# Performance work log

Measured on AMD Instinct MI355X. Metric: run time of the kernel, lower is better.

The kernel has to match this reference:

```python
import jax, jax.numpy as jnp
import numpy as np


def _window_indices(L, K):
    # 0-based (emo, cau) index pairs kept in the torch flattening order:
    # emo varies slowly (outer), cau varies fast (inner), |cau-emo| <= K.
    i = np.repeat(np.arange(L), L)
    j = np.tile(np.arange(L), L)
    m = np.abs(j - i) <= K
    return i[m], j[m]


def setup_inputs() -> dict:
    key = jax.random.key(0)
    ks = jax.random.split(key, 6)
    B, L, D = 4, 512, 768
    K, P = 10, 50
    R = 2 * D + P  # rank_feat_dim = 1586
    return {
        "doc_sents_h": jax.random.normal(ks[0], (B, L, D), jnp.float32),
        "pos_emb": jax.random.normal(ks[1], (2 * K + 1, P), jnp.float32) * 0.05,
        "W1": jax.random.normal(ks[2], (R, R), jnp.float32) * (1.0 / np.sqrt(R)),
        "b1": jax.random.normal(ks[3], (R,), jnp.float32) * 0.01,
        "W2": jax.random.normal(ks[4], (R, 1), jnp.float32) * (1.0 / np.sqrt(R)),
        "b2": jax.random.normal(ks[5], (1,), jnp.float32) * 0.01,
    }


def reference(doc_sents_h, pos_emb, W1, b1, W2, b2):
    B, L, D = doc_sents_h.shape
    K = (pos_emb.shape[0] - 1) // 2
    ei, ci = _window_indices(L, K)           # static numpy, shape [n]
    rel = jnp.asarray(ci - ei)               # [n] in [-K, K]
    # windowed pair features, [B, n, 2D] (skips the O(L^2) materialization)
    P_pairs = jnp.concatenate([doc_sents_h[:, ei], doc_sents_h[:, ci]], axis=-1)
    emb = pos_emb[rel + K]                   # [n, pos_dim]
    relf = rel.astype(pos_emb.dtype)
    kernel = jnp.exp(-jnp.square(relf[:, None] - relf[None, :]))  # [n, n]
    emb = kernel @ emb                       # [n, pos_dim], batch-invariant
    couples = jnp.concatenate(
        [P_pairs, jnp.broadcast_to(emb, (B,) + emb.shape)], axis=-1)  # [B, n, R]
    h = jax.nn.relu(couples @ W1 + b1)       # [B, n, R]
    pred = (h @ W2 + b2)[..., 0]             # [B, n]
    emo_cau_pos = jnp.stack(
        [jnp.asarray(ei) + 1, jnp.asarray(ci) + 1], axis=1)  # [n, 2], 1-based
    return pred, emo_cau_pos, h
```

## Files before the change

kernel.cpp:

```cpp
#include <hip/hip_runtime.h>
#include <math.h>

#define B_   4
#define L_   512
#define D_   768
#define K_   10
#define P_   50
#define R_   1586
#define NP_  10642
#define MROWS 2048
#define NPAD 1664
#define UVS  1600

#define PRED_OFF 0
#define POS_OFF  (B_ * NP_)
#define H_OFF    (B_ * NP_ + NP_ * 2)

typedef __attribute__((ext_vector_type(8))) short short8;
typedef __attribute__((ext_vector_type(4))) float floatx4;

__device__ __forceinline__ unsigned short f2bf(float f) {
    union { float f; unsigned int u; } a; a.f = f;
    unsigned int u = a.u;
    return (unsigned short)((u + 0x7FFF + ((u >> 16) & 1)) >> 16);
}
__device__ __forceinline__ float bf2f(unsigned short u) {
    union { unsigned int u; float f; } a; a.u = ((unsigned int)u) << 16;
    return a.f;
}

__device__ __forceinline__ int pair_offset(int i) {
    int h = i < K_ ? i : K_;
    int off = h * (K_ + 1) + (h * (h - 1)) / 2;
    if (i > K_) {
        int fullEnd = i < (L_ - K_) ? i : (L_ - K_);
        off += (fullEnd - K_) * (2 * K_ + 1);
        if (i > L_ - K_) {
            int t = i - (L_ - K_);
            int first = 2 * K_;
            int last = L_ + K_ - (i - 1);
            off += (first + last) * t / 2;
        }
    }
    return off;
}

#define CA_BLOCKS 1536
#define CW_BLOCKS 2496
__global__ __launch_bounds__(256) void prep(
        const float* __restrict__ doc, const float* __restrict__ pos_emb,
        const float* __restrict__ W1, const float* __restrict__ b1,
        unsigned short* __restrict__ At, unsigned short* __restrict__ Wt,
        unsigned short* __restrict__ Fb) {
    __shared__ float tile[32][33];
    __shared__ float Es[P_];
    const int bid = blockIdx.x;

    if (bid < CA_BLOCKS) {
        int idx = (bid * 256 + threadIdx.x) * 4;
        float4 v = *(const float4*)(doc + idx);
        ushort4 o;
        o.x = f2bf(v.x); o.y = f2bf(v.y); o.z = f2bf(v.z); o.w = f2bf(v.w);
        *(ushort4*)(At + idx) = o;
        return;
    }
    if (bid < CA_BLOCKS + CW_BLOCKS) {
        int bb = bid - CA_BLOCKS;
        int z = bb / 1248, rem = bb % 1248;
        int k0 = (rem % 24) * 32;
        int n0 = (rem / 24) * 32;
        int tx = threadIdx.x & 31, ty = threadIdx.x >> 5;
        #pragma unroll
        for (int r = 0; r < 4; ++r) {
            int k = k0 + ty + r * 8;
            int n = n0 + tx;
            tile[ty + r * 8][tx] = (n < R_) ? W1[(size_t)(z * D_ + k) * R_ + n] : 0.f;
        }
        __syncthreads();
        #pragma unroll
        for (int r = 0; r < 4; ++r) {
            int n = n0 + ty + r * 8;
            int k = k0 + tx;
            Wt[(size_t)z * NPAD * D_ + (size_t)n * D_ + k] = f2bf(tile[tx][ty + r * 8]);
        }
        return;
    }
    int s = bid - (CA_BLOCKS + CW_BLOCKS);
    if (threadIdx.x < P_) {
        float acc = 0.f;
        #pragma unroll
        for (int r = 0; r <= 2 * K_; ++r) {
            float cnt = (float)(L_ - (r > K_ ? r - K_ : K_ - r));
            float d = (float)(s - r);
            acc += cnt * expf(-d * d) * pos_emb[r * P_ + threadIdx.x];
        }
        Es[threadIdx.x] = acc;
    }
    __syncthreads();
    for (int j = threadIdx.x; j < R_; j += 256) {
        float acc = b1[j];
        #pragma unroll 10
        for (int p = 0; p < P_; ++p)
            acc += Es[p] * W1[(2 * D_ + p) * R_ + j];
        Fb[s * UVS + j] = f2bf(acc);
    }
}

#define GLOAD_LDS16(g, l) __builtin_amdgcn_global_load_lds( \
    (const __attribute__((address_space(1))) void*)(g), \
    (__attribute__((address_space(3))) void*)(l), 16, 0, 0)

__global__ __launch_bounds__(256) void gemm_mfma(
        const unsigned short* __restrict__ At,
        const unsigned short* __restrict__ Wt,
        unsigned short* __restrict__ U, unsigned short* __restrict__ V) {
    __shared__ unsigned short Alds[128 * 32];
    __shared__ unsigned short Blds[128 * 32];
    const int tileN = blockIdx.x * 128;
    const int tileM = blockIdx.y * 128;
    const unsigned short* Bt = Wt + (size_t)blockIdx.z * NPAD * D_;
    unsigned short* C = blockIdx.z ? V : U;

    const int lane = threadIdx.x & 63;
    const int w = threadIdx.x >> 6;
    const int wm = (w & 1) * 64, wn = (w >> 1) * 64;
    const int quad = lane >> 4, l16 = lane & 15;

    floatx4 acc[4][4] = {};

    for (int k0 = 0; k0 < D_; k0 += 32) {
        #pragma unroll
        for (int t = 0; t < 2; ++t) {
            int g = (t * 4 + w) * 64 + lane;
            int m = g >> 2, c = g & 3;
            GLOAD_LDS16(At + (size_t)(tileM + m) * D_ + k0 + c * 8,
                        Alds + (t * 4 + w) * 512);
            GLOAD_LDS16(Bt + (size_t)(tileN + m) * D_ + k0 + c * 8,
                        Blds + (t * 4 + w) * 512);
        }
        __syncthreads();
        short8 a[4], b[4];
        #pragma unroll
        for (int im = 0; im < 4; ++im)
            a[im] = *(const short8*)&Alds[(wm + im * 16 + l16) * 32 + quad * 8];
        #pragma unroll
        for (int in = 0; in < 4; ++in)
            b[in] = *(const short8*)&Blds[(wn + in * 16 + l16) * 32 + quad * 8];
        #pragma unroll
        for (int im = 0; im < 4; ++im)
            #pragma unroll
            for (int in = 0; in < 4; ++in)
                acc[im][in] = __builtin_amdgcn_mfma_f32_16x16x32_bf16(
                    a[im], b[in], acc[im][in], 0, 0, 0);
        __syncthreads();
    }
    #pragma unroll
    for (int im = 0; im < 4; ++im) {
        #pragma unroll
        for (int in = 0; in < 4; ++in) {
            int col = tileN + wn + in * 16 + l16;
            if (col < R_) {
                #pragma unroll
                for (int r = 0; r < 4; ++r) {
                    int row = tileM + wm + im * 16 + quad * 4 + r;
                    C[(size_t)row * UVS + col] = f2bf(acc[im][in][r]);
                }
            }
        }
    }
}

#define NC2 13
__global__ __launch_bounds__(256) void epilogue(
        const unsigned short* __restrict__ U, const unsigned short* __restrict__ V,
        const unsigned short* __restrict__ Fb, const float* __restrict__ W2,
        const float* __restrict__ b2, float* __restrict__ out) {
    const int w    = threadIdx.x >> 6;
    const int lane = threadIdx.x & 63;
    const int b    = blockIdx.x >> 9;
    const int i    = blockIdx.x & (L_ - 1);

    const ushort2* u2  = (const ushort2*)(U + (size_t)(b * L_ + i) * UVS);
    const float2*  w2v = (const float2*)W2;

    float2 ur[NC2], wr[NC2];
    #pragma unroll
    for (int t = 0; t < NC2; ++t) {
        int c = lane + t * 64;
        if (c < R_ / 2) {
            ushort2 uu = u2[c];
            ur[t] = make_float2(bf2f(uu.x), bf2f(uu.y));
            wr[t] = w2v[c];
        }
    }

    const int base = i - K_ > 0 ? i - K_ : 0;
    const int poff = pair_offset(i);
    const float bias = b2[0];

    for (int dj = w; dj < 2 * K_ + 1; dj += 4) {
        int j = i - K_ + dj;
        if ((unsigned)j >= L_) continue;
        int p = poff + (j - base);
        const ushort2* v2 = (const ushort2*)(V + (size_t)(b * L_ + j) * UVS);
        const ushort2* f2 = (const ushort2*)(Fb + (size_t)dj * UVS);
        double* h2 = (double*)(out + H_OFF + (size_t)(b * NP_ + p) * R_);

        float acc = 0.f;
        #pragma unroll
        for (int t = 0; t < NC2; ++t) {
            int c = lane + t * 64;
            if (c < R_ / 2) {
                ushort2 vv = v2[c], ff = f2[c];
                float h0 = fmaxf(ur[t].x + bf2f(vv.x) + bf2f(ff.x), 0.f);
                float h1 = fmaxf(ur[t].y + bf2f(vv.y) + bf2f(ff.y), 0.f);
                union { float2 f; double d; } pk;
                pk.f = make_float2(h0, h1);
                __builtin_nontemporal_store(pk.d, h2 + c);
                acc += h0 * wr[t].x + h1 * wr[t].y;
            }
        }
        #pragma unroll
        for (int off = 32; off; off >>= 1) acc += __shfl_down(acc, off, 64);
        if (lane == 0) {
            out[PRED_OFF + b * NP_ + p] = acc + bias;
            if (b == 0) {
                out[POS_OFF + p * 2 + 0] = (float)(i + 1);
                out[POS_OFF + p * 2 + 1] = (float)(j + 1);
            }
        }
    }
}

extern "C" void kernel_launch(void* const* d_in, const int* in_sizes, int n_in,
                              void* d_out, int out_size, void* d_ws, size_t ws_size,
                              hipStream_t stream) {
    const float* doc     = (const float*)d_in[0];
    const float* pos_emb = (const float*)d_in[1];
    const float* W1      = (const float*)d_in[2];
    const float* b1      = (const float*)d_in[3];
    const float* W2      = (const float*)d_in[4];
    const float* b2      = (const float*)d_in[5];
    float* out = (float*)d_out;

    char* ws = (char*)d_ws;
    size_t off = 0;
    unsigned short* U  = (unsigned short*)(ws + off); off += (size_t)MROWS * UVS * 2;
    unsigned short* V  = (unsigned short*)(ws + off); off += (size_t)MROWS * UVS * 2;
    unsigned short* Fb = (unsigned short*)(ws + off); off += (size_t)21 * UVS * 2;
    off = (off + 255) & ~(size_t)255;
    unsigned short* At = (unsigned short*)(ws + off); off += (size_t)MROWS * D_ * 2;
    off = (off + 255) & ~(size_t)255;
    unsigned short* Wt = (unsigned short*)(ws + off);

    prep<<<CA_BLOCKS + CW_BLOCKS + 21, 256, 0, stream>>>(
        doc, pos_emb, W1, b1, At, Wt, Fb);
    gemm_mfma<<<dim3(NPAD / 128, MROWS / 128, 2), 256, 0, stream>>>(At, Wt, U, V);
    epilogue<<<dim3(MROWS), 256, 0, stream>>>(U, V, Fb, W2, b2, out);
}
```

Before: 361.1 us.

## Double-buffer LDS tiles in MFMA GEMM to overlap global loads with compute

The GEMM kernel now uses two LDS buffers for the A and B tiles. It issues the global-to-LDS loads for the next K-step before running the MFMAs on the current one, using explicit vmcnt waits and barriers. This is meant to hide global memory latency behind the matrix math instead of stalling on every K iteration. In exchange it doubles LDS use per block, which may lower occupancy, and it depends on hand-written waitcnt counts being correct.

```diff
diff --git a/kernel.cpp b/kernel.cpp
--- a/kernel.cpp
+++ b/kernel.cpp
@@ -114,8 +114,8 @@
         const unsigned short* __restrict__ At,
         const unsigned short* __restrict__ Wt,
         unsigned short* __restrict__ U, unsigned short* __restrict__ V) {
-    __shared__ unsigned short Alds[128 * 32];
-    __shared__ unsigned short Blds[128 * 32];
+    __shared__ unsigned short Alds[2][128 * 32];
+    __shared__ unsigned short Blds[2][128 * 32];
     const int tileN = blockIdx.x * 128;
     const int tileM = blockIdx.y * 128;
     const unsigned short* Bt = Wt + (size_t)blockIdx.z * NPAD * D_;
@@ -128,32 +128,51 @@
 
     floatx4 acc[4][4] = {};
 
-    for (int k0 = 0; k0 < D_; k0 += 32) {
-        #pragma unroll
-        for (int t = 0; t < 2; ++t) {
-            int g = (t * 4 + w) * 64 + lane;
-            int m = g >> 2, c = g & 3;
-            GLOAD_LDS16(At + (size_t)(tileM + m) * D_ + k0 + c * 8,
-                        Alds + (t * 4 + w) * 512);
-            GLOAD_LDS16(Bt + (size_t)(tileN + m) * D_ + k0 + c * 8,
-                        Blds + (t * 4 + w) * 512);
-        }
-        __syncthreads();
-        short8 a[4], b[4];
-        #pragma unroll
-        for (int im = 0; im < 4; ++im)
-            a[im] = *(const short8*)&Alds[(wm + im * 16 + l16) * 32 + quad * 8];
-        #pragma unroll
-        for (int in = 0; in < 4; ++in)
-            b[in] = *(const short8*)&Blds[(wn + in * 16 + l16) * 32 + quad * 8];
-        #pragma unroll
-        for (int im = 0; im < 4; ++im)
-            #pragma unroll
-            for (int in = 0; in < 4; ++in)
-                acc[im][in] = __builtin_amdgcn_mfma_f32_16x16x32_bf16(
-                    a[im], b[in], acc[im][in], 0, 0, 0);
-        __syncthreads();
-    }
+#define STAGE(buf, kk) do { \
+        _Pragma("unroll") \
+        for (int t = 0; t < 2; ++t) { \
+            int g = (t * 4 + w) * 64 + lane; \
+            int m = g >> 2, c = g & 3; \
+            GLOAD_LDS16(At + (size_t)(tileM + m) * D_ + (kk) + c * 8, \
+                        &Alds[buf][(t * 4 + w) * 512]); \
+            GLOAD_LDS16(Bt + (size_t)(tileN + m) * D_ + (kk) + c * 8, \
+                        &Blds[buf][(t * 4 + w) * 512]); \
+        } } while (0)
+
+#define KSTEP(rb, kk, dopf) do { \
+        if (dopf) { \
+            STAGE(rb ^ 1, (kk) + 32); \
+            asm volatile("s_waitcnt vmcnt(4)" ::: "memory"); \
+        } else { \
+            asm volatile("s_waitcnt vmcnt(0)" ::: "memory"); \
+        } \
+        __builtin_amdgcn_s_barrier(); \
+        __builtin_amdgcn_sched_barrier(0); \
+        short8 a[4], b[4]; \
+        _Pragma("unroll") \
+        for (int im = 0; im < 4; ++im) \
+            a[im] = *(const short8*)&Alds[rb][(wm + im * 16 + l16) * 32 + quad * 8]; \
+        _Pragma("unroll") \
+        for (int in = 0; in < 4; ++in) \
+            b[in] = *(const short8*)&Blds[rb][(wn + in * 16 + l16) * 32 + quad * 8]; \
+        _Pragma("unroll") \
+        for (int im = 0; im < 4; ++im) \
+            _Pragma("unroll") \
+            for (int in = 0; in < 4; ++in) \
+                acc[im][in] = __builtin_amdgcn_mfma_f32_16x16x32_bf16( \
+                    a[im], b[in], acc[im][in], 0, 0, 0); \
+        __builtin_amdgcn_sched_barrier(0); \
+        __builtin_amdgcn_s_barrier(); \
+    } while (0)
+
+    STAGE(0, 0);
+    for (int k0 = 0; k0 < D_; k0 += 64) {
+        KSTEP(0, k0, true);
+        KSTEP(1, k0 + 32, (k0 + 64) < D_);
+    }
+#undef KSTEP
+#undef STAGE
+
     #pragma unroll
     for (int im = 0; im < 4; ++im) {
         #pragma unroll
```

New measurement: 363.6 us. No clear change (+0.7%).

## Fuse prep, GEMM and epilogue into one cooperative persistent kernel

Applied to the files above, without the earlier changes.

Merges the three kernels into a single cooperative launch of 416 blocks. A grid-stride loop covers the prep jobs, grid.sync separates the phases, and one GEMM tile is assigned per block. The goal is to remove two kernel launch gaps and the tail idle time between dependent kernels. In exchange, occupancy is capped at 2 blocks per CU with combined LDS, and grid-wide barriers are added. The epilogue also runs with fewer resident blocks than its original 2048-block launch.

```diff
diff --git a/kernel.cpp b/kernel.cpp
--- a/kernel.cpp
+++ b/kernel.cpp
@@ -1,5 +1,8 @@
 #include <hip/hip_runtime.h>
+#include <hip/hip_cooperative_groups.h>
 #include <math.h>
+
+namespace cg = cooperative_groups;
 
 #define B_   4
 #define L_   512
@@ -15,6 +18,8 @@
 #define PRED_OFF 0
 #define POS_OFF  (B_ * NP_)
 #define H_OFF    (B_ * NP_ + NP_ * 2)
+
+#define GRID_ 416
 
 typedef __attribute__((ext_vector_type(8))) short short8;
 typedef __attribute__((ext_vector_type(4))) float floatx4;
@@ -47,186 +52,193 @@
 
 #define CA_BLOCKS 1536
 #define CW_BLOCKS 2496
-__global__ __launch_bounds__(256) void prep(
-        const float* __restrict__ doc, const float* __restrict__ pos_emb,
-        const float* __restrict__ W1, const float* __restrict__ b1,
-        unsigned short* __restrict__ At, unsigned short* __restrict__ Wt,
-        unsigned short* __restrict__ Fb) {
-    __shared__ float tile[32][33];
-    __shared__ float Es[P_];
-    const int bid = blockIdx.x;
-
-    if (bid < CA_BLOCKS) {
-        int idx = (bid * 256 + threadIdx.x) * 4;
-        float4 v = *(const float4*)(doc + idx);
-        ushort4 o;
-        o.x = f2bf(v.x); o.y = f2bf(v.y); o.z = f2bf(v.z); o.w = f2bf(v.w);
-        *(ushort4*)(At + idx) = o;
-        return;
-    }
-    if (bid < CA_BLOCKS + CW_BLOCKS) {
-        int bb = bid - CA_BLOCKS;
-        int z = bb / 1248, rem = bb % 1248;
-        int k0 = (rem % 24) * 32;
-        int n0 = (rem / 24) * 32;
-        int tx = threadIdx.x & 31, ty = threadIdx.x >> 5;
-        #pragma unroll
-        for (int r = 0; r < 4; ++r) {
-            int k = k0 + ty + r * 8;
-            int n = n0 + tx;
-            tile[ty + r * 8][tx] = (n < R_) ? W1[(size_t)(z * D_ + k) * R_ + n] : 0.f;
-        }
-        __syncthreads();
-        #pragma unroll
-        for (int r = 0; r < 4; ++r) {
-            int n = n0 + ty + r * 8;
-            int k = k0 + tx;
-            Wt[(size_t)z * NPAD * D_ + (size_t)n * D_ + k] = f2bf(tile[tx][ty + r * 8]);
-        }
-        return;
-    }
-    int s = bid - (CA_BLOCKS + CW_BLOCKS);
-    if (threadIdx.x < P_) {
-        float acc = 0.f;
-        #pragma unroll
-        for (int r = 0; r <= 2 * K_; ++r) {
-            float cnt = (float)(L_ - (r > K_ ? r - K_ : K_ - r));
-            float d = (float)(s - r);
-            acc += cnt * expf(-d * d) * pos_emb[r * P_ + threadIdx.x];
-        }
-        Es[threadIdx.x] = acc;
-    }
-    __syncthreads();
-    for (int j = threadIdx.x; j < R_; j += 256) {
-        float acc = b1[j];
-        #pragma unroll 10
-        for (int p = 0; p < P_; ++p)
-            acc += Es[p] * W1[(2 * D_ + p) * R_ + j];
-        Fb[s * UVS + j] = f2bf(acc);
-    }
-}
+#define PREP_JOBS (CA_BLOCKS + CW_BLOCKS + 21)
 
 #define GLOAD_LDS16(g, l) __builtin_amdgcn_global_load_lds( \
     (const __attribute__((address_space(1))) void*)(g), \
     (__attribute__((address_space(3))) void*)(l), 16, 0, 0)
 
-__global__ __launch_bounds__(256) void gemm_mfma(
-        const unsigned short* __restrict__ At,
-        const unsigned short* __restrict__ Wt,
-        unsigned short* __restrict__ U, unsigned short* __restrict__ V) {
+#define NC2 13
+
+__global__ __launch_bounds__(256, 2) void fused(
+        const float* __restrict__ doc, const float* __restrict__ pos_emb,
+        const float* __restrict__ W1, const float* __restrict__ b1,
+        const float* __restrict__ W2, const float* __restrict__ b2,
+        unsigned short* __restrict__ At, unsigned short* __restrict__ Wt,
+        unsigned short* __restrict__ Fb, unsigned short* __restrict__ U,
+        unsigned short* __restrict__ V, float* __restrict__ out) {
+    __shared__ float tile[32][33];
+    __shared__ float Es[P_];
     __shared__ unsigned short Alds[128 * 32];
     __shared__ unsigned short Blds[128 * 32];
-    const int tileN = blockIdx.x * 128;
-    const int tileM = blockIdx.y * 128;
-    const unsigned short* Bt = Wt + (size_t)blockIdx.z * NPAD * D_;
-    unsigned short* C = blockIdx.z ? V : U;
-
+
+    cg::grid_group grid = cg::this_grid();
+    const int bid  = blockIdx.x;
     const int lane = threadIdx.x & 63;
-    const int w = threadIdx.x >> 6;
-    const int wm = (w & 1) * 64, wn = (w >> 1) * 64;
-    const int quad = lane >> 4, l16 = lane & 15;
-
-    floatx4 acc[4][4] = {};
-
-    for (int k0 = 0; k0 < D_; k0 += 32) {
+    const int w    = threadIdx.x >> 6;
+
+    for (int job = bid; job < PREP_JOBS; job += GRID_) {
+        if (job < CA_BLOCKS) {
+            int idx = (job * 256 + threadIdx.x) * 4;
+            float4 v = *(const float4*)(doc + idx);
+            ushort4 o;
+            o.x = f2bf(v.x); o.y = f2bf(v.y); o.z = f2bf(v.z); o.w = f2bf(v.w);
+            *(ushort4*)(At + idx) = o;
+        } else if (job < CA_BLOCKS + CW_BLOCKS) {
+            int bb = job - CA_BLOCKS;
+            int z = bb / 1248, rem = bb % 1248;
+            int k0 = (rem % 24) * 32;
+            int n0 = (rem / 24) * 32;
+            int tx = threadIdx.x & 31, ty = threadIdx.x >> 5;
+            #pragma unroll
+            for (int r = 0; r < 4; ++r) {
+                int k = k0 + ty + r * 8;
+                int n = n0 + tx;
+                tile[ty + r * 8][tx] = (n < R_) ? W1[(size_t)(z * D_ + k) * R_ + n] : 0.f;
+            }
+            __syncthreads();
+            #pragma unroll
+            for (int r = 0; r < 4; ++r) {
+                int n = n0 + ty + r * 8;
+                int k = k0 + tx;
+                Wt[(size_t)z * NPAD * D_ + (size_t)n * D_ + k] = f2bf(tile[tx][ty + r * 8]);
+            }
+            __syncthreads();
+        } else {
+            int s = job - (CA_BLOCKS + CW_BLOCKS);
+            if (threadIdx.x < P_) {
+                float acc = 0.f;
+                #pragma unroll
+                for (int r = 0; r <= 2 * K_; ++r) {
+                    float cnt = (float)(L_ - (r > K_ ? r - K_ : K_ - r));
+                    float d = (float)(s - r);
+                    acc += cnt * expf(-d * d) * pos_emb[r * P_ + threadIdx.x];
+                }
+                Es[threadIdx.x] = acc;
+            }
+            __syncthreads();
+            for (int j = threadIdx.x; j < R_; j += 256) {
+                float acc = b1[j];
+                #pragma unroll 10
+                for (int p = 0; p < P_; ++p)
+                    acc += Es[p] * W1[(2 * D_ + p) * R_ + j];
+                Fb[s * UVS + j] = f2bf(acc);
+            }
+            __syncthreads();
+        }
+    }
+
+    grid.sync();
+
+    {
+        const int z   = bid / 208;
+        const int rem = bid % 208;
+        const int tileM = (rem / 13) * 128;
+        const int tileN = (rem % 13) * 128;
+        const unsigned short* Bt = Wt + (size_t)z * NPAD * D_;
+        unsigned short* C = z ? V : U;
+
+        const int wm = (w & 1) * 64, wn = (w >> 1) * 64;
+        const int quad = lane >> 4, l16 = lane & 15;
+
+        floatx4 acc[4][4] = {};
+
+        for (int k0 = 0; k0 < D_; k0 += 32) {
+            #pragma unroll
+            for (int t = 0; t < 2; ++t) {
+                int g = (t * 4 + w) * 64 + lane;
+                int m = g >> 2, c = g & 3;
+                GLOAD_LDS16(At + (size_t)(tileM + m) * D_ + k0 + c * 8,
+                            Alds + (t * 4 + w) * 512);
+                GLOAD_LDS16(Bt + (size_t)(tileN + m) * D_ + k0 + c * 8,
+                            Blds + (t * 4 + w) * 512);
+            }
+            __syncthreads();
+            short8 a[4], b[4];
+            #pragma unroll
+            for (int im = 0; im < 4; ++im)
+                a[im] = *(const short8*)&Alds[(wm + im * 16 + l16) * 32 + quad * 8];
+            #pragma unroll
+            for (int in = 0; in < 4; ++in)
+                b[in] = *(const short8*)&Blds[(wn + in * 16 + l16) * 32 + quad * 8];
+            #pragma unroll
+            for (int im = 0; im < 4; ++im)
+                #pragma unroll
+                for (int in = 0; in < 4; ++in)
+                    acc[im][in] = __builtin_amdgcn_mfma_f32_16x16x32_bf16(
+                        a[im], b[in], acc[im][in], 0, 0, 0);
+            __syncthreads();
+        }
         #pragma unroll
-        for (int t = 0; t < 2; ++t) {
-            int g = (t * 4 + w) * 64 + lane;
-            int m = g >> 2, c = g & 3;
-            GLOAD_LDS16(At + (size_t)(tileM + m) * D_ + k0 + c * 8,
-                        Alds + (t * 4 + w) * 512);
-            GLOAD_LDS16(Bt + (size_t)(tileN + m) * D_ + k0 + c * 8,
-                        Blds + (t * 4 + w) * 512);
-        }
-        __syncthreads();
-        short8 a[4], b[4];
-        #pragma unroll
-        for (int im = 0; im < 4; ++im)
-            a[im] = *(const short8*)&Alds[(wm + im * 16 + l16) * 32 + quad * 8];
-        #pragma unroll
-        for (int in = 0; in < 4; ++in)
-            b[in] = *(const short8*)&Blds[(wn + in * 16 + l16) * 32 + quad * 8];
-        #pragma unroll
-        for (int im = 0; im < 4; ++im)
-            #pragma unroll
-            for (int in = 0; in < 4; ++in)
-                acc[im][in] = __builtin_amdgcn_mfma_f32_16x16x32_bf16(
-                    a[im], b[in], acc[im][in], 0, 0, 0);
-        __syncthreads();
-    }
-    #pragma unroll
-    for (int im = 0; im < 4; ++im) {
-        #pragma unroll
-        for (int in = 0; in < 4; ++in) {
-            int col = tileN + wn + in * 16 + l16;
-            if (col < R_) {
-                #pragma unroll
-                for (int r = 0; r < 4; ++r) {
-                    int row = tileM + wm + im * 16 + quad * 4 + r;
-                    C[(size_t)row * UVS + col] = f2bf(acc[im][in][r]);
-                }
-            }
-        }
-    }
-}
-
-#define NC2 13
-__global__ __launch_bounds__(256) void epilogue(
-        const unsigned short* __restrict__ U, const unsigned short* __restrict__ V,
-        const unsigned short* __restrict__ Fb, const float* __restrict__ W2,
-        const float* __restrict__ b2, float* __restrict__ out) {
-    const int w    = threadIdx.x >> 6;
-    const int lane = threadIdx.x & 63;
-    const int b    = blockIdx.x >> 9;
-    const int i    = blockIdx.x & (L_ - 1);
-
-    const ushort2* u2  = (const ushort2*)(U + (size_t)(b * L_ + i) * UVS);
-    const float2*  w2v = (const float2*)W2;
-
-    float2 ur[NC2], wr[NC2];
-    #pragma unroll
-    for (int t = 0; t < NC2; ++t) {
-        int c = lane + t * 64;
-        if (c < R_ / 2) {
-            ushort2 uu = u2[c];
-            ur[t] = make_float2(bf2f(uu.x), bf2f(uu.y));
-            wr[t] = w2v[c];
-        }
-    }
-
-    const int base = i - K_ > 0 ? i - K_ : 0;
-    const int poff = pair_offset(i);
-    const float bias = b2[0];
-
-    for (int dj = w; dj < 2 * K_ + 1; dj += 4) {
-        int j = i - K_ + dj;
-        if ((unsigned)j >= L_) continue;
-        int p = poff + (j - base);
-        const ushort2* v2 = (const ushort2*)(V + (size_t)(b * L_ + j) * UVS);
-        const ushort2* f2 = (const ushort2*)(Fb + (size_t)dj * UVS);
-        double* h2 = (double*)(out + H_OFF + (size_t)(b * NP_ + p) * R_);
-
-        float acc = 0.f;
+        for (int im = 0; im < 4; ++im) {
+            #pragma unroll
+            for (int in = 0; in < 4; ++in) {
+                int col = tileN + wn + in * 16 + l16;
+                if (col < R_) {
+                    #pragma unroll
+                    for (int r = 0; r < 4; ++r) {
+                        int row = tileM + wm + im * 16 + quad * 4 + r;
+                        C[(size_t)row * UVS + col] = f2bf(acc[im][in][r]);
+                    }
+                }
+            }
+        }
+    }
+
+    grid.sync();
+
+    for (int job = bid; job < MROWS; job += GRID_) {
+        const int b = job >> 9;
+        const int i = job & (L_ - 1);
+
+        const ushort2* u2  = (const ushort2*)(U + (size_t)(b * L_ + i) * UVS);
+        const float2*  w2v = (const float2*)W2;
+
+        float2 ur[NC2], wr[NC2];
         #pragma unroll
         for (int t = 0; t < NC2; ++t) {
             int c = lane + t * 64;
             if (c < R_ / 2) {
-                ushort2 vv = v2[c], ff = f2[c];
-                float h0 = fmaxf(ur[t].x + bf2f(vv.x) + bf2f(ff.x), 0.f);
-                float h1 = fmaxf(ur[t].y + bf2f(vv.y) + bf2f(ff.y), 0.f);
-                union { float2 f; double d; } pk;
-                pk.f = make_float2(h0, h1);
-                __builtin_nontemporal_store(pk.d, h2 + c);
-                acc += h0 * wr[t].x + h1 * wr[t].y;
-            }
-        }
-        #pragma unroll
-        for (int off = 32; off; off >>= 1) acc += __shfl_down(acc, off, 64);
-        if (lane == 0) {
-            out[PRED_OFF + b * NP_ + p] = acc + bias;
-            if (b == 0) {
-                out[POS_OFF + p * 2 + 0] = (float)(i + 1);
-                out[POS_OFF + p * 2 + 1] = (float)(j + 1);
+                ushort2 uu = u2[c];
+                ur[t] = make_float2(bf2f(uu.x), bf2f(uu.y));
+                wr[t] = w2v[c];
+            }
+        }
+
+        const int base = i - K_ > 0 ? i - K_ : 0;
+        const int poff = pair_offset(i);
+        const float bias = b2[0];
+
+        for (int dj = w; dj < 2 * K_ + 1; dj += 4) {
+            int j = i - K_ + dj;
+            if ((unsigned)j >= L_) continue;
+            int p = poff + (j - base);
+            const ushort2* v2 = (const ushort2*)(V + (size_t)(b * L_ + j) * UVS);
+            const ushort2* f2 = (const ushort2*)(Fb + (size_t)dj * UVS);
+            double* h2 = (double*)(out + H_OFF + (size_t)(b * NP_ + p) * R_);
+
+            float acc = 0.f;
+            #pragma unroll
+            for (int t = 0; t < NC2; ++t) {
+                int c = lane + t * 64;
+                if (c < R_ / 2) {
+                    ushort2 vv = v2[c], ff = f2[c];
+                    float h0 = fmaxf(ur[t].x + bf2f(vv.x) + bf2f(ff.x), 0.f);
+                    float h1 = fmaxf(ur[t].y + bf2f(vv.y) + bf2f(ff.y), 0.f);
+                    union { float2 f; double d; } pk;
+                    pk.f = make_float2(h0, h1);
+                    __builtin_nontemporal_store(pk.d, h2 + c);
+                    acc += h0 * wr[t].x + h1 * wr[t].y;
+                }
+            }
+            #pragma unroll
+            for (int off = 32; off; off >>= 1) acc += __shfl_down(acc, off, 64);
+            if (lane == 0) {
+                out[PRED_OFF + b * NP_ + p] = acc + bias;
+                if (b == 0) {
+                    out[POS_OFF + p * 2 + 0] = (float)(i + 1);
+                    out[POS_OFF + p * 2 + 1] = (float)(j + 1);
+                }
             }
         }
     }
@@ -253,8 +265,9 @@
     off = (off + 255) & ~(size_t)255;
     unsigned short* Wt = (unsigned short*)(ws + off);
 
-    prep<<<CA_BLOCKS + CW_BLOCKS + 21, 256, 0, stream>>>(
-        doc, pos_emb, W1, b1, At, Wt, Fb);
-    gemm_mfma<<<dim3(NPAD / 128, MROWS / 128, 2), 256, 0, stream>>>(At, Wt, U, V);
-    epilogue<<<dim3(MROWS), 256, 0, stream>>>(U, V, Fb, W2, b2, out);
-}
+    void* args[] = { (void*)&doc, (void*)&pos_emb, (void*)&W1, (void*)&b1,
+                     (void*)&W2, (void*)&b2, (void*)&At, (void*)&Wt,
+                     (void*)&Fb, (void*)&U, (void*)&V, (void*)&out };
+    hipLaunchCooperativeKernel((const void*)fused, dim3(GRID_), dim3(256),
+                               args, 0, stream);
+}
```

Result: slower. 1.002 ms (+177.4%).
